# Performance work log

Hardware: AMD Instinct MI355X
Metric: run time of the kernel (lower is better)

The kernel has to match this reference:

```python
import jax, jax.numpy as jnp
import numpy as np

N = 10000        # nodes
E = 320000       # edges (before self-loops)
IN = 128         # in_channels
HID = 128        # hidden_channels per head
HEADS = 4
OUT = 512        # out_channels (final layer, 1 head, no concat)
SLOPE = 0.2      # PyG GATConv negative_slope default


def setup_inputs() -> dict:
    key = jax.random.key(0)
    ks = jax.random.split(key, 16)
    s = 0.05
    inp = {
        "x": jax.random.normal(ks[0], (N, IN), dtype=jnp.float32),
        "edge_index": jax.random.randint(ks[1], (2, E), 0, N, dtype=jnp.int32),
        # layer 1: IN -> HEADS*HID, concat
        "W1": jax.random.normal(ks[2], (IN, HEADS * HID), dtype=jnp.float32) * s,
        "a_src1": jax.random.normal(ks[3], (1, HEADS, HID), dtype=jnp.float32) * s,
        "a_dst1": jax.random.normal(ks[4], (1, HEADS, HID), dtype=jnp.float32) * s,
        "b1": jnp.zeros((HEADS * HID,), dtype=jnp.float32),
        # layer 2: HEADS*HID -> HEADS*HID, concat
        "W2": jax.random.normal(ks[5], (HEADS * HID, HEADS * HID), dtype=jnp.float32) * s,
        "a_src2": jax.random.normal(ks[6], (1, HEADS, HID), dtype=jnp.float32) * s,
        "a_dst2": jax.random.normal(ks[7], (1, HEADS, HID), dtype=jnp.float32) * s,
        "b2": jnp.zeros((HEADS * HID,), dtype=jnp.float32),
        # layer 3: HEADS*HID -> OUT, heads=1, mean (no concat)
        "W3": jax.random.normal(ks[8], (HEADS * HID, OUT), dtype=jnp.float32) * s,
        "a_src3": jax.random.normal(ks[9], (1, 1, OUT), dtype=jnp.float32) * s,
        "a_dst3": jax.random.normal(ks[10], (1, 1, OUT), dtype=jnp.float32) * s,
        "b3": jnp.zeros((OUT,), dtype=jnp.float32),
    }
    return inp


def gat_layer(x, src, dst, W, a_src, a_dst, bias, heads, ch, concat):
    n = x.shape[0]
    h = (x @ W).reshape(n, heads, ch)                 # [N,H,C]
    al_s = jnp.sum(h * a_src, axis=-1)                # [N,H]
    al_d = jnp.sum(h * a_dst, axis=-1)                # [N,H]
    logits = jax.nn.leaky_relu(al_s[src] + al_d[dst], SLOPE)  # [E,H]
    # segment softmax over incoming edges of each destination node
    logits = logits - jax.ops.segment_max(logits, dst, num_segments=n)[dst]
    e = jnp.exp(logits)
    denom = jax.ops.segment_sum(e, dst, num_segments=n)[dst]
    alpha = e / denom                                  # [E,H]
    out = jax.ops.segment_sum(h[src] * alpha[:, :, None], dst, num_segments=n)  # [N,H,C]
    out = out.reshape(n, heads * ch) if concat else out.mean(axis=1)
    return out + bias


def reference(x, edge_index, W1, a_src1, a_dst1, b1, W2, a_src2, a_dst2, b2,
              W3, a_src3, a_dst3, b3):
    n = x.shape[0]
    loop = jnp.arange(n, dtype=edge_index.dtype)       # PyG add_self_loops=True
    src = jnp.concatenate([edge_index[0], loop])
    dst = jnp.concatenate([edge_index[1], loop])
    h = jax.nn.relu(gat_layer(x, src, dst, W1, a_src1, a_dst1, b1, HEADS, HID, True))
    h = jax.nn.relu(gat_layer(h, src, dst, W2, a_src2, a_dst2, b2, HEADS, HID, True))
    return gat_layer(h, src, dst, W3, a_src3, a_dst3, b3, 1, OUT, False)
```

## Files before the change

kernel.cpp:

```cpp
#include <hip/hip_runtime.h>

#define NSLOPE 0.2f
#define CAP 128

typedef __bf16 bf16x8 __attribute__((ext_vector_type(8)));
typedef __bf16 bf16x4 __attribute__((ext_vector_type(4)));
typedef __bf16 bf16x2 __attribute__((ext_vector_type(2)));
typedef float  f32x4  __attribute__((ext_vector_type(4)));
typedef _Float16 half2v __attribute__((ext_vector_type(2)));

static __device__ __forceinline__ float dot2f(unsigned p, unsigned a, float c){
#if __has_builtin(__builtin_amdgcn_fdot2)
  return __builtin_amdgcn_fdot2(__builtin_bit_cast(half2v, p),
                                __builtin_bit_cast(half2v, a), c, false);
#else
  half2v ph = __builtin_bit_cast(half2v, p), ah = __builtin_bit_cast(half2v, a);
  return c + (float)ph[0]*(float)ah[0] + (float)ph[1]*(float)ah[1];
#endif
}


__global__ void fill_kernel(const int* __restrict__ ei, int E,
                            int* cnt, int* __restrict__ col){
  int i = blockIdx.x*blockDim.x + threadIdx.x;
  if (i < E){
    int s = ei[i], d = ei[E + i];
    int slot = atomicAdd(&cnt[d], 1);
    if (slot < CAP) col[(d << 7) + slot] = s;
  }
}

__device__ __forceinline__ void wsplit_body(
    const float* __restrict__ W, __bf16* __restrict__ Bt, int K, int Nc,
    int kb, int nb, float (*hi_s)[33]){
  int tx = threadIdx.x & 31, ty = threadIdx.x >> 5;
  int k0 = kb * 32, n0 = nb * 32;
#pragma unroll
  for (int i = 0; i < 4; i++){
    int r = ty + i*8;
    hi_s[r][tx] = (float)(__bf16)W[(size_t)(k0 + r)*Nc + n0 + tx];
  }
  __syncthreads();
  const size_t Kx16 = (size_t)K * 16;
#pragma unroll
  for (int i = 0; i < 4; i++){
    int n = ty + i*8;
    int r = n0 + n;
    size_t a = (size_t)(r >> 4)*Kx16 + (size_t)(k0 >> 5)*512
             + (size_t)((r & 15) + 16*(tx >> 3))*8 + (tx & 7);
    Bt[a] = (__bf16)hi_s[tx][n];
  }
}

__global__ __launch_bounds__(256) void prep_kernel(
    const float* __restrict__ x, __bf16* __restrict__ X2,
    const float* __restrict__ W1, __bf16* __restrict__ B1t,
    const float* __restrict__ W2, __bf16* __restrict__ B2t,
    const float* __restrict__ W3, __bf16* __restrict__ B3t,
    int* __restrict__ cnt, int* __restrict__ col,
    float* __restrict__ albase, int N){
  __shared__ float hi_s[32][33];
  int b = blockIdx.x, t = threadIdx.x;
  int gid = b*256 + t;
  if (gid < N){
    cnt[gid] = 1;
    col[gid << 7] = gid;
  }
  if (gid*4 < N*18) *(float4*)(albase + gid*4) = make_float4(0.f,0.f,0.f,0.f);

  const int nb_split = (N*32 + 255) / 256;
  if (b < nb_split){
    int i = gid * 4;
    if (i < N*128){
      int n = i >> 7, c = i & 127;
      float4 v = *(const float4*)(x + i);
      float f[4] = {v.x, v.y, v.z, v.w};
      bf16x4 h;
#pragma unroll
      for (int u = 0; u < 4; u++) h[u] = (__bf16)f[u];
      size_t a = (size_t)(n >> 4)*2048 + (size_t)(c >> 5)*512
               + (size_t)((n & 15) + 16*((c >> 3) & 3))*8 + (c & 7);
      *(bf16x4*)(X2 + a) = h;
    }
  } else if (b < nb_split + 64){
    int bb = b - nb_split;
    wsplit_body(W1, B1t, 128, 512, bb & 3, bb >> 2, hi_s);
  } else if (b < nb_split + 64 + 256){
    int bb = b - nb_split - 64;
    wsplit_body(W2, B2t, 512, 512, bb & 15, bb >> 4, hi_s);
  } else {
    int bb = b - nb_split - 320;
    wsplit_body(W3, B3t, 512, 512, bb & 15, bb >> 4, hi_s);
  }
}

template<int H>
__global__ __launch_bounds__(256) void gemm_mfma(
    const __bf16* __restrict__ A2f, const __bf16* __restrict__ B2f,
    _Float16* __restrict__ Hb, const float* __restrict__ asrc,
    const float* __restrict__ adst, float* __restrict__ al_s,
    float* __restrict__ al_d, int M, int K2){
  int t = threadIdx.x, w = t >> 6, lane = t & 63;
  int mm = lane & 15, q = lane >> 4;

  int bid = blockIdx.x;
  int idx = bid >> 3;
  int cb = idx & 3;
  int rowblk = (bid & 7) + ((idx >> 2) << 3);
  if (rowblk * 64 >= M) return;
  int bm = rowblk * 64, bn = cb * 128;
  int wr = w & 1, wc = w >> 1;

  const int nf = K2 >> 5;
  const int rbmax = (M >> 4) - 1;
  const __bf16* pA0; const __bf16* pA1;
  const __bf16* pB0; const __bf16* pB1; const __bf16* pB2; const __bf16* pB3;
  {
    int rb0 = (bm >> 4) + wr*2;     rb0 = (rb0 <= rbmax) ? rb0 : rbmax;
    int rb1 = (bm >> 4) + wr*2 + 1; rb1 = (rb1 <= rbmax) ? rb1 : rbmax;
    pA0 = A2f + (size_t)rb0*nf*512 + lane*8;
    pA1 = A2f + (size_t)rb1*nf*512 + lane*8;
    int rbB = (bn >> 4) + wc*4;
    pB0 = B2f + (size_t)(rbB+0)*nf*512 + lane*8;
    pB1 = B2f + (size_t)(rbB+1)*nf*512 + lane*8;
    pB2 = B2f + (size_t)(rbB+2)*nf*512 + lane*8;
    pB3 = B2f + (size_t)(rbB+3)*nf*512 + lane*8;
  }

  f32x4 acc[2][4];
#pragma unroll
  for (int i = 0; i < 2; i++)
#pragma unroll
    for (int j = 0; j < 4; j++)
#pragma unroll
      for (int r = 0; r < 4; r++) acc[i][j][r] = 0.f;

#pragma unroll 4
  for (int f = 0; f < nf; f++){
    bf16x8 a0 = *(const bf16x8*)(pA0 + (size_t)f*512);
    bf16x8 a1 = *(const bf16x8*)(pA1 + (size_t)f*512);
    bf16x8 b0 = *(const bf16x8*)(pB0 + (size_t)f*512);
    bf16x8 b1 = *(const bf16x8*)(pB1 + (size_t)f*512);
    bf16x8 b2 = *(const bf16x8*)(pB2 + (size_t)f*512);
    bf16x8 b3 = *(const bf16x8*)(pB3 + (size_t)f*512);
    acc[0][0] = __builtin_amdgcn_mfma_f32_16x16x32_bf16(a0, b0, acc[0][0], 0, 0, 0);
    acc[0][1] = __builtin_amdgcn_mfma_f32_16x16x32_bf16(a0, b1, acc[0][1], 0, 0, 0);
    acc[0][2] = __builtin_amdgcn_mfma_f32_16x16x32_bf16(a0, b2, acc[0][2], 0, 0, 0);
    acc[0][3] = __builtin_amdgcn_mfma_f32_16x16x32_bf16(a0, b3, acc[0][3], 0, 0, 0);
    acc[1][0] = __builtin_amdgcn_mfma_f32_16x16x32_bf16(a1, b0, acc[1][0], 0, 0, 0);
    acc[1][1] = __builtin_amdgcn_mfma_f32_16x16x32_bf16(a1, b1, acc[1][1], 0, 0, 0);
    acc[1][2] = __builtin_amdgcn_mfma_f32_16x16x32_bf16(a1, b2, acc[1][2], 0, 0, 0);
    acc[1][3] = __builtin_amdgcn_mfma_f32_16x16x32_bf16(a1, b3, acc[1][3], 0, 0, 0);
  }

  float as_v[4], ad_v[4];
#pragma unroll
  for (int j2 = 0; j2 < 4; j2++){
    int colc = bn + (wc*4 + j2)*16 + mm;
    as_v[j2] = asrc[colc];
    ad_v[j2] = adst[colc];
  }
  const int h = (H == 4) ? (bn >> 7) : 0;
#pragma unroll
  for (int i2 = 0; i2 < 2; i2++){
    int rbase = bm + (wr*2 + i2)*16 + q*4;
#pragma unroll
    for (int j2 = 0; j2 < 4; j2++){
      int colc = bn + (wc*4 + j2)*16 + mm;
#pragma unroll
      for (int r = 0; r < 4; r++){
        int row = rbase + r;
        if (row < M) Hb[(size_t)row*512 + colc] = (_Float16)acc[i2][j2][r];
      }
    }
#pragma unroll
    for (int r = 0; r < 4; r++){
      float ps = acc[i2][0][r]*as_v[0] + acc[i2][1][r]*as_v[1]
               + acc[i2][2][r]*as_v[2] + acc[i2][3][r]*as_v[3];
      float pd = acc[i2][0][r]*ad_v[0] + acc[i2][1][r]*ad_v[1]
               + acc[i2][2][r]*ad_v[2] + acc[i2][3][r]*ad_v[3];
#pragma unroll
      for (int off = 1; off < 16; off <<= 1){
        ps += __shfl_xor(ps, off);
        pd += __shfl_xor(pd, off);
      }
      int row = rbase + r;
      if (mm == 0 && row < M){
        atomicAdd(&al_s[(size_t)row*H + h], ps);
        atomicAdd(&al_d[(size_t)row*H + h], pd);
      }
    }
  }
}

template<int H, int MODE>
__global__ __launch_bounds__(256) void aggregate_slice(
    const _Float16* __restrict__ Hb, const float* __restrict__ al_s,
    const float* __restrict__ al_d, const int* __restrict__ cnt,
    const int* __restrict__ col, const float* __restrict__ bias,
    float* __restrict__ outF, __bf16* __restrict__ fA,
    int nidx, int N){
  __shared__ int      src_s[4][64];
  __shared__ _Float16 a_sh[4][64];
  int g = blockIdx.x;
  int x = g & 7, grp = g >> 3;
  int s = x >> 1, half = x & 1;
  int t = threadIdx.x, w = t >> 6, lane = t & 63;
  int dd = grp*4 + w;
  if (dd >= nidx) return;
  int d = half * nidx + dd;
  if (d >= N) return;
  const int hh = (H == 1) ? 0 : s;
  const float ald = al_d[(size_t)d*H + hh];
  int deg = cnt[d]; deg = (deg < CAP) ? deg : CAP;
  int start = d << 7;

  int sc0 = 0, sc1 = 0;
  float v0f = -1e30f, v1f = -1e30f;
  if (lane < deg){
    sc0 = col[start + lane];
    float v = al_s[(size_t)sc0*H + hh] + ald;
    v0f = (v > 0.f) ? v : NSLOPE * v;
  }
  if (64 + lane < deg){
    sc1 = col[start + 64 + lane];
    float v = al_s[(size_t)sc1*H + hh] + ald;
    v1f = (v > 0.f) ? v : NSLOPE * v;
  }
  float mx = fmaxf(v0f, v1f);
#pragma unroll
  for (int off = 32; off > 0; off >>= 1)
    mx = fmaxf(mx, __shfl_xor(mx, off));

  float e0 = (lane < deg)      ? __expf(v0f - mx) : 0.f;
  float e1 = (64 + lane < deg) ? __expf(v1f - mx) : 0.f;
  float lsum = e0 + e1;
#pragma unroll
  for (int off = 32; off > 0; off >>= 1)
    lsum += __shfl_xor(lsum, off);

  const unsigned* __restrict__ Hb32 = (const unsigned*)Hb;
  const unsigned coffu = s*64 + lane;
  float accx = 0.f, accy = 0.f;

  int cc0 = (deg < 64) ? deg : 64;
  src_s[w][lane] = sc0;
  a_sh[w][lane]  = (_Float16)e0;
  for (int chunk = 0; ; chunk++){
    int cnt2 = (chunk == 0) ? cc0 : (deg - 64);
    int npair = cnt2 >> 1;
    int j = 0;
    for (; j + 2 <= npair; j += 2){
      int s0 = src_s[w][2*j],     s1 = src_s[w][2*j+1];
      int s2 = src_s[w][2*j+2],   s3 = src_s[w][2*j+3];
      unsigned a01 = *(const unsigned*)&a_sh[w][2*j];
      unsigned a23 = *(const unsigned*)&a_sh[w][2*j+2];
      unsigned u0 = Hb32[(size_t)s0*256 + coffu];
      unsigned u1 = Hb32[(size_t)s1*256 + coffu];
      unsigned u2 = Hb32[(size_t)s2*256 + coffu];
      unsigned u3 = Hb32[(size_t)s3*256 + coffu];
      unsigned pc  = (u0 & 0x0000ffffu) | (u1 << 16);
      unsigned pc1 = (u0 >> 16) | (u1 & 0xffff0000u);
      unsigned qc  = (u2 & 0x0000ffffu) | (u3 << 16);
      unsigned qc1 = (u2 >> 16) | (u3 & 0xffff0000u);
      accx = dot2f(pc,  a01, accx);
      accy = dot2f(pc1, a01, accy);
      accx = dot2f(qc,  a23, accx);
      accy = dot2f(qc1, a23, accy);
    }
    for (; j < npair; j++){
      int s0 = src_s[w][2*j], s1 = src_s[w][2*j+1];
      unsigned a01 = *(const unsigned*)&a_sh[w][2*j];
      unsigned u0 = Hb32[(size_t)s0*256 + coffu];
      unsigned u1 = Hb32[(size_t)s1*256 + coffu];
      unsigned pc  = (u0 & 0x0000ffffu) | (u1 << 16);
      unsigned pc1 = (u0 >> 16) | (u1 & 0xffff0000u);
      accx = dot2f(pc,  a01, accx);
      accy = dot2f(pc1, a01, accy);
    }
    if (cnt2 & 1){
      int sl = src_s[w][cnt2 - 1];
      float al = (float)a_sh[w][cnt2 - 1];
      unsigned ul = Hb32[(size_t)sl*256 + coffu];
      half2v hv = __builtin_bit_cast(half2v, ul);
      accx += al * (float)hv[0];
      accy += al * (float)hv[1];
    }
    if (chunk == 1 || deg <= 64) break;
    src_s[w][lane] = sc1;
    a_sh[w][lane]  = (_Float16)e1;
  }

  float invd = 1.f / lsum;
  int c = s*128 + lane*2;
  float2 bv = *(const float2*)(bias + c);
  float r0 = accx * invd + bv.x;
  float r1 = accy * invd + bv.y;
  if (MODE == 1){
    r0 = fmaxf(r0, 0.f); r1 = fmaxf(r1, 0.f);
    bf16x2 hv; hv[0] = (__bf16)r0; hv[1] = (__bf16)r1;
    size_t a = (size_t)(d >> 4)*8192 + (size_t)(c >> 5)*512
             + (size_t)((d & 15) + 16*((c >> 3) & 3))*8 + (c & 7);
    *(bf16x2*)(fA + a) = hv;
  } else {
    *(float2*)(outF + (size_t)d*512 + c) = make_float2(r0, r1);
  }
}

extern "C" void kernel_launch(void* const* d_in, const int* in_sizes, int n_in,
                              void* d_out, int out_size, void* d_ws, size_t ws_size,
                              hipStream_t stream){
  const float* x   = (const float*)d_in[0];
  const int*   ei  = (const int*)  d_in[1];
  const float* W1  = (const float*)d_in[2];
  const float* as1 = (const float*)d_in[3];
  const float* ad1 = (const float*)d_in[4];
  const float* b1  = (const float*)d_in[5];
  const float* W2  = (const float*)d_in[6];
  const float* as2 = (const float*)d_in[7];
  const float* ad2 = (const float*)d_in[8];
  const float* b2  = (const float*)d_in[9];
  const float* W3  = (const float*)d_in[10];
  const float* as3 = (const float*)d_in[11];
  const float* ad3 = (const float*)d_in[12];
  const float* b3  = (const float*)d_in[13];
  float* out = (float*)d_out;

  const int N = in_sizes[0] / 128;
  const int E = in_sizes[1] / 2;
  const int nidx = (N + 1) / 2;

  __bf16* feat2  = (__bf16*)d_ws;
  __bf16* X2     = feat2 + (size_t)N*512;
  float*  albase = (float*)(X2 + (size_t)N*128);
  float*  als1   = albase;
  float*  ald1   = als1 + (size_t)N*4;
  float*  als2   = ald1 + (size_t)N*4;
  float*  ald2   = als2 + (size_t)N*4;
  float*  als3   = ald2 + (size_t)N*4;
  float*  ald3   = als3 + (size_t)N;
  int*    cnt    = (int*)(ald3 + (size_t)N);
  int*    col    = cnt + N;
  uintptr_t p  = (uintptr_t)(col + (size_t)N*CAP);
  p = (p + 15) & ~(uintptr_t)15;
  __bf16* B1t = (__bf16*)p;
  __bf16* B2t = B1t + 512*128;
  __bf16* B3t = B2t + 512*512;
  _Float16* Hb = (_Float16*)(B3t + 512*512);

  const int nb_split = (N*32 + 255)/256;
  const int pgrid = nb_split + 64 + 256 + 256;

  prep_kernel<<<pgrid, 256, 0, stream>>>(x, X2, W1, B1t, W2, B2t, W3, B3t,
                                         cnt, col, albase, N);
  fill_kernel<<<(E+255)/256, 256, 0, stream>>>(ei, E, cnt, col);

  const int nrb = (N + 63)/64;
  const int ggrid = (((nrb + 7) >> 3) << 3) * 4;
  const int agrid = ((nidx + 3)/4) * 8;

  gemm_mfma<4><<<ggrid, 256, 0, stream>>>(X2, B1t, Hb, as1, ad1, als1, ald1, N, 128);
  aggregate_slice<4,1><<<agrid, 256, 0, stream>>>(Hb, als1, ald1, cnt, col, b1,
      (float*)nullptr, feat2, nidx, N);

  gemm_mfma<4><<<ggrid, 256, 0, stream>>>(feat2, B2t, Hb, as2, ad2, als2, ald2, N, 512);
  aggregate_slice<4,1><<<agrid, 256, 0, stream>>>(Hb, als2, ald2, cnt, col, b2,
      (float*)nullptr, feat2, nidx, N);

  gemm_mfma<1><<<ggrid, 256, 0, stream>>>(feat2, B3t, Hb, as3, ad3, als3, ald3, N, 512);
  aggregate_slice<1,0><<<agrid, 256, 0, stream>>>(Hb, als3, ald3, cnt, col, b3,
      out, (__bf16*)nullptr, nidx, N);
}
```

Baseline: 272.6 us.

## Fuse all GAT stages into one persistent cooperative kernel with grid syncs

Replaces the eight separate kernel launches (prep, fill, three GEMM and three aggregation kernels) with a single cooperative mega-kernel. Each phase loops over virtual block indices and is separated from the next by grid.sync(). The aim is to remove launch gaps and per-kernel tail effects between the dependent stages. In exchange, occupancy is limited by the combined register and shared-memory footprint of all phases. Grid-wide barriers add cost, and the launch falls back to separate kernels if the cooperative launch fails.

```diff
diff --git a/kernel.cpp b/kernel.cpp
--- a/kernel.cpp
+++ b/kernel.cpp
@@ -1,4 +1,6 @@
 #include <hip/hip_runtime.h>
+#include <hip/hip_cooperative_groups.h>
+namespace cg = cooperative_groups;
 
 #define NSLOPE 0.2f
 #define CAP 128
@@ -20,15 +22,18 @@
 }
 
 
-__global__ void fill_kernel(const int* __restrict__ ei, int E,
-                            int* cnt, int* __restrict__ col){
-  int i = blockIdx.x*blockDim.x + threadIdx.x;
-  if (i < E){
-    int s = ei[i], d = ei[E + i];
-    int slot = atomicAdd(&cnt[d], 1);
-    if (slot < CAP) col[(d << 7) + slot] = s;
-  }
-}
+struct MegaP {
+  const float* x; const int* ei;
+  const float* W1; const float* as1; const float* ad1; const float* b1;
+  const float* W2; const float* as2; const float* ad2; const float* b2;
+  const float* W3; const float* as3; const float* ad3; const float* b3;
+  float* out;
+  __bf16* feat2; __bf16* X2; float* albase;
+  float* als1; float* ald1; float* als2; float* ald2; float* als3; float* ald3;
+  int* cnt; int* col;
+  __bf16* B1t; __bf16* B2t; __bf16* B3t; _Float16* Hb;
+  int N, E, nidx;
+};
 
 __device__ __forceinline__ void wsplit_body(
     const float* __restrict__ W, __bf16* __restrict__ Bt, int K, int Nc,
@@ -52,58 +57,60 @@
   }
 }
 
-__global__ __launch_bounds__(256) void prep_kernel(
-    const float* __restrict__ x, __bf16* __restrict__ X2,
-    const float* __restrict__ W1, __bf16* __restrict__ B1t,
-    const float* __restrict__ W2, __bf16* __restrict__ B2t,
-    const float* __restrict__ W3, __bf16* __restrict__ B3t,
-    int* __restrict__ cnt, int* __restrict__ col,
-    float* __restrict__ albase, int N){
-  __shared__ float hi_s[32][33];
-  int b = blockIdx.x, t = threadIdx.x;
+__device__ __forceinline__ void prep_body(int b, int t, const MegaP& p,
+                                          float (*hi_s)[33]){
+  const int N = p.N;
   int gid = b*256 + t;
   if (gid < N){
-    cnt[gid] = 1;
-    col[gid << 7] = gid;
-  }
-  if (gid*4 < N*18) *(float4*)(albase + gid*4) = make_float4(0.f,0.f,0.f,0.f);
+    p.cnt[gid] = 1;
+    p.col[gid << 7] = gid;
+  }
+  if (gid*4 < N*18) *(float4*)(p.albase + gid*4) = make_float4(0.f,0.f,0.f,0.f);
 
   const int nb_split = (N*32 + 255) / 256;
   if (b < nb_split){
     int i = gid * 4;
     if (i < N*128){
       int n = i >> 7, c = i & 127;
-      float4 v = *(const float4*)(x + i);
+      float4 v = *(const float4*)(p.x + i);
       float f[4] = {v.x, v.y, v.z, v.w};
       bf16x4 h;
 #pragma unroll
       for (int u = 0; u < 4; u++) h[u] = (__bf16)f[u];
       size_t a = (size_t)(n >> 4)*2048 + (size_t)(c >> 5)*512
                + (size_t)((n & 15) + 16*((c >> 3) & 3))*8 + (c & 7);
-      *(bf16x4*)(X2 + a) = h;
+      *(bf16x4*)(p.X2 + a) = h;
     }
   } else if (b < nb_split + 64){
     int bb = b - nb_split;
-    wsplit_body(W1, B1t, 128, 512, bb & 3, bb >> 2, hi_s);
+    wsplit_body(p.W1, p.B1t, 128, 512, bb & 3, bb >> 2, hi_s);
   } else if (b < nb_split + 64 + 256){
     int bb = b - nb_split - 64;
-    wsplit_body(W2, B2t, 512, 512, bb & 15, bb >> 4, hi_s);
-  } else {
+    wsplit_body(p.W2, p.B2t, 512, 512, bb & 15, bb >> 4, hi_s);
+  } else if (b < nb_split + 64 + 512){
     int bb = b - nb_split - 320;
-    wsplit_body(W3, B3t, 512, 512, bb & 15, bb >> 4, hi_s);
+    wsplit_body(p.W3, p.B3t, 512, 512, bb & 15, bb >> 4, hi_s);
+  }
+}
+
+__device__ __forceinline__ void fill_body(int b, int t, const MegaP& p){
+  int i = b*256 + t;
+  if (i < p.E){
+    int s = p.ei[i], d = p.ei[p.E + i];
+    int slot = atomicAdd(&p.cnt[d], 1);
+    if (slot < CAP) p.col[(d << 7) + slot] = s;
   }
 }
 
 template<int H>
-__global__ __launch_bounds__(256) void gemm_mfma(
+__device__ __forceinline__ void gemm_body(int bid, int t,
     const __bf16* __restrict__ A2f, const __bf16* __restrict__ B2f,
     _Float16* __restrict__ Hb, const float* __restrict__ asrc,
     const float* __restrict__ adst, float* __restrict__ al_s,
     float* __restrict__ al_d, int M, int K2){
-  int t = threadIdx.x, w = t >> 6, lane = t & 63;
+  int w = t >> 6, lane = t & 63;
   int mm = lane & 15, q = lane >> 4;
 
-  int bid = blockIdx.x;
   int idx = bid >> 3;
   int cb = idx & 3;
   int rowblk = (bid & 7) + ((idx >> 2) << 3);
@@ -194,18 +201,15 @@
 }
 
 template<int H, int MODE>
-__global__ __launch_bounds__(256) void aggregate_slice(
+__device__ __forceinline__ void agg_body(int g, int t,
     const _Float16* __restrict__ Hb, const float* __restrict__ al_s,
     const float* __restrict__ al_d, const int* __restrict__ cnt,
     const int* __restrict__ col, const float* __restrict__ bias,
-    float* __restrict__ outF, __bf16* __restrict__ fA,
-    int nidx, int N){
-  __shared__ int      src_s[4][64];
-  __shared__ _Float16 a_sh[4][64];
-  int g = blockIdx.x;
+    float* __restrict__ outF, __bf16* __restrict__ fA, int nidx, int N,
+    int (*src_s)[64], _Float16 (*a_sh)[64]){
   int x = g & 7, grp = g >> 3;
   int s = x >> 1, half = x & 1;
-  int t = threadIdx.x, w = t >> 6, lane = t & 63;
+  int w = t >> 6, lane = t & 63;
   int dd = grp*4 + w;
   if (dd >= nidx) return;
   int d = half * nidx + dd;
@@ -307,25 +311,79 @@
   }
 }
 
+__global__ __launch_bounds__(256) void mega(MegaP p){
+  cg::grid_group grid = cg::this_grid();
+  __shared__ float hi_s[32][33];
+  __shared__ int src_s[4][64];
+  __shared__ _Float16 a_sh[4][64];
+  const int G = gridDim.x, b0 = blockIdx.x, t = threadIdx.x;
+  const int N = p.N, E = p.E, nidx = p.nidx;
+
+  const int nb_split = (N*32 + 255)/256;
+  const int pgrid = nb_split + 64 + 256 + 256;
+  for (int b = b0; b < pgrid; b += G){
+    prep_body(b, t, p, hi_s);
+    __syncthreads();
+  }
+  grid.sync();
+  const int fgrid = (E + 255)/256;
+  for (int b = b0; b < fgrid; b += G) fill_body(b, t, p);
+  grid.sync();
+
+  const int nrb = (N + 63)/64;
+  const int ggrid = (((nrb + 7) >> 3) << 3) * 4;
+  const int agrid = ((nidx + 3)/4) * 8;
+
+  for (int b = b0; b < ggrid; b += G)
+    gemm_body<4>(b, t, p.X2, p.B1t, p.Hb, p.as1, p.ad1, p.als1, p.ald1, N, 128);
+  grid.sync();
+  for (int b = b0; b < agrid; b += G)
+    agg_body<4,1>(b, t, p.Hb, p.als1, p.ald1, p.cnt, p.col, p.b1,
+                  (float*)nullptr, p.feat2, nidx, N, src_s, a_sh);
+  grid.sync();
+  for (int b = b0; b < ggrid; b += G)
+    gemm_body<4>(b, t, p.feat2, p.B2t, p.Hb, p.as2, p.ad2, p.als2, p.ald2, N, 512);
+  grid.sync();
+  for (int b = b0; b < agrid; b += G)
+    agg_body<4,1>(b, t, p.Hb, p.als2, p.ald2, p.cnt, p.col, p.b2,
+                  (float*)nullptr, p.feat2, nidx, N, src_s, a_sh);
+  grid.sync();
+  for (int b = b0; b < ggrid; b += G)
+    gemm_body<1>(b, t, p.feat2, p.B3t, p.Hb, p.as3, p.ad3, p.als3, p.ald3, N, 512);
+  grid.sync();
+  for (int b = b0; b < agrid; b += G)
+    agg_body<1,0>(b, t, p.Hb, p.als3, p.ald3, p.cnt, p.col, p.b3,
+                  p.out, (__bf16*)nullptr, nidx, N, src_s, a_sh);
+}
+
+__global__ __launch_bounds__(256) void prep_kernel(MegaP p){
+  __shared__ float hi_s[32][33];
+  prep_body(blockIdx.x, threadIdx.x, p, hi_s);
+}
+__global__ void fill_kernel(MegaP p){
+  fill_body(blockIdx.x, threadIdx.x, p);
+}
+template<int H>
+__global__ __launch_bounds__(256) void gemm_k(
+    const __bf16* A2f, const __bf16* B2f, _Float16* Hb,
+    const float* asrc, const float* adst, float* al_s, float* al_d,
+    int M, int K2){
+  gemm_body<H>(blockIdx.x, threadIdx.x, A2f, B2f, Hb, asrc, adst, al_s, al_d, M, K2);
+}
+template<int H, int MODE>
+__global__ __launch_bounds__(256) void agg_k(
+    const _Float16* Hb, const float* al_s, const float* al_d,
+    const int* cnt, const int* col, const float* bias,
+    float* outF, __bf16* fA, int nidx, int N){
+  __shared__ int src_s[4][64];
+  __shared__ _Float16 a_sh[4][64];
+  agg_body<H,MODE>(blockIdx.x, threadIdx.x, Hb, al_s, al_d, cnt, col, bias,
+                   outF, fA, nidx, N, src_s, a_sh);
+}
+
 extern "C" void kernel_launch(void* const* d_in, const int* in_sizes, int n_in,
                               void* d_out, int out_size, void* d_ws, size_t ws_size,
                               hipStream_t stream){
-  const float* x   = (const float*)d_in[0];
-  const int*   ei  = (const int*)  d_in[1];
-  const float* W1  = (const float*)d_in[2];
-  const float* as1 = (const float*)d_in[3];
-  const float* ad1 = (const float*)d_in[4];
-  const float* b1  = (const float*)d_in[5];
-  const float* W2  = (const float*)d_in[6];
-  const float* as2 = (const float*)d_in[7];
-  const float* ad2 = (const float*)d_in[8];
-  const float* b2  = (const float*)d_in[9];
-  const float* W3  = (const float*)d_in[10];
-  const float* as3 = (const float*)d_in[11];
-  const float* ad3 = (const float*)d_in[12];
-  const float* b3  = (const float*)d_in[13];
-  float* out = (float*)d_out;
-
   const int N = in_sizes[0] / 128;
   const int E = in_sizes[1] / 2;
   const int nidx = (N + 1) / 2;
@@ -341,33 +399,58 @@
   float*  ald3   = als3 + (size_t)N;
   int*    cnt    = (int*)(ald3 + (size_t)N);
   int*    col    = cnt + N;
-  uintptr_t p  = (uintptr_t)(col + (size_t)N*CAP);
-  p = (p + 15) & ~(uintptr_t)15;
-  __bf16* B1t = (__bf16*)p;
+  uintptr_t pa = (uintptr_t)(col + (size_t)N*CAP);
+  pa = (pa + 15) & ~(uintptr_t)15;
+  __bf16* B1t = (__bf16*)pa;
   __bf16* B2t = B1t + 512*128;
   __bf16* B3t = B2t + 512*512;
   _Float16* Hb = (_Float16*)(B3t + 512*512);
 
-  const int nb_split = (N*32 + 255)/256;
-  const int pgrid = nb_split + 64 + 256 + 256;
-
-  prep_kernel<<<pgrid, 256, 0, stream>>>(x, X2, W1, B1t, W2, B2t, W3, B3t,
-                                         cnt, col, albase, N);
-  fill_kernel<<<(E+255)/256, 256, 0, stream>>>(ei, E, cnt, col);
-
-  const int nrb = (N + 63)/64;
-  const int ggrid = (((nrb + 7) >> 3) << 3) * 4;
-  const int agrid = ((nidx + 3)/4) * 8;
-
-  gemm_mfma<4><<<ggrid, 256, 0, stream>>>(X2, B1t, Hb, as1, ad1, als1, ald1, N, 128);
-  aggregate_slice<4,1><<<agrid, 256, 0, stream>>>(Hb, als1, ald1, cnt, col, b1,
-      (float*)nullptr, feat2, nidx, N);
-
-  gemm_mfma<4><<<ggrid, 256, 0, stream>>>(feat2, B2t, Hb, as2, ad2, als2, ald2, N, 512);
-  aggregate_slice<4,1><<<agrid, 256, 0, stream>>>(Hb, als2, ald2, cnt, col, b2,
-      (float*)nullptr, feat2, nidx, N);
-
-  gemm_mfma<1><<<ggrid, 256, 0, stream>>>(feat2, B3t, Hb, as3, ad3, als3, ald3, N, 512);
-  aggregate_slice<1,0><<<agrid, 256, 0, stream>>>(Hb, als3, ald3, cnt, col, b3,
-      out, (__bf16*)nullptr, nidx, N);
-}
+  MegaP P;
+  P.x = (const float*)d_in[0];   P.ei = (const int*)d_in[1];
+  P.W1 = (const float*)d_in[2];  P.as1 = (const float*)d_in[3];
+  P.ad1 = (const float*)d_in[4]; P.b1 = (const float*)d_in[5];
+  P.W2 = (const float*)d_in[6];  P.as2 = (const float*)d_in[7];
+  P.ad2 = (const float*)d_in[8]; P.b2 = (const float*)d_in[9];
+  P.W3 = (const float*)d_in[10]; P.as3 = (const float*)d_in[11];
+  P.ad3 = (const float*)d_in[12]; P.b3 = (const float*)d_in[13];
+  P.out = (float*)d_out;
+  P.feat2 = feat2; P.X2 = X2; P.albase = albase;
+  P.als1 = als1; P.ald1 = ald1; P.als2 = als2; P.ald2 = ald2;
+  P.als3 = als3; P.ald3 = ald3;
+  P.cnt = cnt; P.col = col;
+  P.B1t = B1t; P.B2t = B2t; P.B3t = B3t; P.Hb = Hb;
+  P.N = N; P.E = E; P.nidx = nidx;
+
+  int maxb = 0;
+  hipError_t oe = hipOccupancyMaxActiveBlocksPerMultiprocessor(
+      &maxb, reinterpret_cast<const void*>(mega), 256, 0);
+  if (oe != hipSuccess || maxb < 1) maxb = 2;
+  long Gl = (long)maxb * 256;
+  if (Gl > 2048) Gl = 2048;
+  int G = (int)(Gl & ~7L);
+  if (G < 256) G = 256;
+
+  void* kargs[] = { &P };
+  hipError_t le = hipLaunchCooperativeKernel(
+      reinterpret_cast<const void*>(mega), dim3(G), dim3(256), kargs, 0, stream);
+
+  if (le != hipSuccess){
+    const int nb_split = (N*32 + 255)/256;
+    const int pgrid = nb_split + 64 + 256 + 256;
+    prep_kernel<<<pgrid, 256, 0, stream>>>(P);
+    fill_kernel<<<(E+255)/256, 256, 0, stream>>>(P);
+    const int nrb = (N + 63)/64;
+    const int ggrid = (((nrb + 7) >> 3) << 3) * 4;
+    const int agrid = ((nidx + 3)/4) * 8;
+    gemm_k<4><<<ggrid, 256, 0, stream>>>(X2, B1t, Hb, P.as1, P.ad1, als1, ald1, N, 128);
+    agg_k<4,1><<<agrid, 256, 0, stream>>>(Hb, als1, ald1, cnt, col, P.b1,
+        (float*)nullptr, feat2, nidx, N);
+    gemm_k<4><<<ggrid, 256, 0, stream>>>(feat2, B2t, Hb, P.as2, P.ad2, als2, ald2, N, 512);
+    agg_k<4,1><<<agrid, 256, 0, stream>>>(Hb, als2, ald2, cnt, col, P.b2,
+        (float*)nullptr, feat2, nidx, N);
+    gemm_k<1><<<ggrid, 256, 0, stream>>>(feat2, B3t, Hb, P.as3, P.ad3, als3, ald3, N, 512);
+    agg_k<1,0><<<agrid, 256, 0, stream>>>(Hb, als3, ald3, cnt, col, P.b3,
+        P.out, (__bf16*)nullptr, nidx, N);
+  }
+}
```

Result: slower. 873.1 us (+220.3%).

## Split each destination's edge list across four waves with block-level reduction

Applied to the files above, without the earlier changes.

The aggregation kernel now assigns one destination node (and head slice) per block instead of one per wave. Its edge list is divided into four quarters, one per wave, and the softmax max/sum and the accumulators are combined through shared memory with __syncthreads. Source indices and exp weights are broadcast with shuffles instead of LDS arrays, and the weights are packed to fp16 on the fly. The goal is to cut per-wave serial latency over the ~33 edges per node and raise memory-level parallelism. In exchange it launches four times as many blocks, adds barriers, and leaves three of the four waves idle in the epilogue.

```diff
diff --git a/kernel.cpp b/kernel.cpp
--- a/kernel.cpp
+++ b/kernel.cpp
@@ -16,6 +16,15 @@
 #else
   half2v ph = __builtin_bit_cast(half2v, p), ah = __builtin_bit_cast(half2v, a);
   return c + (float)ph[0]*(float)ah[0] + (float)ph[1]*(float)ah[1];
+#endif
+}
+
+static __device__ __forceinline__ unsigned pk2h(float a, float b){
+#if __has_builtin(__builtin_amdgcn_cvt_pkrtz)
+  return __builtin_bit_cast(unsigned, __builtin_amdgcn_cvt_pkrtz(a, b));
+#else
+  half2v h; h[0] = (_Float16)a; h[1] = (_Float16)b;
+  return __builtin_bit_cast(unsigned, h);
 #endif
 }
 
@@ -200,110 +209,105 @@
     const int* __restrict__ col, const float* __restrict__ bias,
     float* __restrict__ outF, __bf16* __restrict__ fA,
     int nidx, int N){
-  __shared__ int      src_s[4][64];
-  __shared__ _Float16 a_sh[4][64];
+  __shared__ float red[8];
+  __shared__ float partx[4][64], party[4][64];
   int g = blockIdx.x;
-  int x = g & 7, grp = g >> 3;
+  int x = g & 7, idx = g >> 3;
   int s = x >> 1, half = x & 1;
+  int d = half * nidx + idx;
+  if (d >= N) return;
   int t = threadIdx.x, w = t >> 6, lane = t & 63;
-  int dd = grp*4 + w;
-  if (dd >= nidx) return;
-  int d = half * nidx + dd;
-  if (d >= N) return;
   const int hh = (H == 1) ? 0 : s;
   const float ald = al_d[(size_t)d*H + hh];
   int deg = cnt[d]; deg = (deg < CAP) ? deg : CAP;
   int start = d << 7;
-
-  int sc0 = 0, sc1 = 0;
-  float v0f = -1e30f, v1f = -1e30f;
-  if (lane < deg){
-    sc0 = col[start + lane];
-    float v = al_s[(size_t)sc0*H + hh] + ald;
-    v0f = (v > 0.f) ? v : NSLOPE * v;
-  }
-  if (64 + lane < deg){
-    sc1 = col[start + 64 + lane];
-    float v = al_s[(size_t)sc1*H + hh] + ald;
-    v1f = (v > 0.f) ? v : NSLOPE * v;
-  }
-  float mx = fmaxf(v0f, v1f);
+  int qlen = (deg + 3) >> 2;
+  int qbeg = w * qlen;
+  int qcnt = deg - qbeg;
+  qcnt = (qcnt < 0) ? 0 : ((qcnt < qlen) ? qcnt : qlen);
+
+  int sc = 0; float vf = -1e30f;
+  if (lane < qcnt){
+    sc = col[start + qbeg + lane];
+    float v = al_s[(size_t)sc*H + hh] + ald;
+    vf = (v > 0.f) ? v : NSLOPE * v;
+  }
+  float mx = vf;
 #pragma unroll
   for (int off = 32; off > 0; off >>= 1)
     mx = fmaxf(mx, __shfl_xor(mx, off));
-
-  float e0 = (lane < deg)      ? __expf(v0f - mx) : 0.f;
-  float e1 = (64 + lane < deg) ? __expf(v1f - mx) : 0.f;
-  float lsum = e0 + e1;
+  if (lane == 0) red[w] = mx;
+  __syncthreads();
+  mx = fmaxf(fmaxf(red[0], red[1]), fmaxf(red[2], red[3]));
+  float e = (lane < qcnt) ? __expf(vf - mx) : 0.f;
+  float ss = e;
 #pragma unroll
   for (int off = 32; off > 0; off >>= 1)
-    lsum += __shfl_xor(lsum, off);
+    ss += __shfl_xor(ss, off);
+  if (lane == 0) red[4 + w] = ss;
+  __syncthreads();
+  float lsum = (red[4] + red[5]) + (red[6] + red[7]);
 
   const unsigned* __restrict__ Hb32 = (const unsigned*)Hb;
   const unsigned coffu = s*64 + lane;
   float accx = 0.f, accy = 0.f;
 
-  int cc0 = (deg < 64) ? deg : 64;
-  src_s[w][lane] = sc0;
-  a_sh[w][lane]  = (_Float16)e0;
-  for (int chunk = 0; ; chunk++){
-    int cnt2 = (chunk == 0) ? cc0 : (deg - 64);
-    int npair = cnt2 >> 1;
-    int j = 0;
-    for (; j + 2 <= npair; j += 2){
-      int s0 = src_s[w][2*j],     s1 = src_s[w][2*j+1];
-      int s2 = src_s[w][2*j+2],   s3 = src_s[w][2*j+3];
-      unsigned a01 = *(const unsigned*)&a_sh[w][2*j];
-      unsigned a23 = *(const unsigned*)&a_sh[w][2*j+2];
-      unsigned u0 = Hb32[(size_t)s0*256 + coffu];
-      unsigned u1 = Hb32[(size_t)s1*256 + coffu];
-      unsigned u2 = Hb32[(size_t)s2*256 + coffu];
-      unsigned u3 = Hb32[(size_t)s3*256 + coffu];
-      unsigned pc  = (u0 & 0x0000ffffu) | (u1 << 16);
-      unsigned pc1 = (u0 >> 16) | (u1 & 0xffff0000u);
-      unsigned qc  = (u2 & 0x0000ffffu) | (u3 << 16);
-      unsigned qc1 = (u2 >> 16) | (u3 & 0xffff0000u);
-      accx = dot2f(pc,  a01, accx);
-      accy = dot2f(pc1, a01, accy);
-      accx = dot2f(qc,  a23, accx);
-      accy = dot2f(qc1, a23, accy);
+  int npc = (qcnt + 1) >> 1;
+  int j = 0;
+  for (; j + 2 <= npc; j += 2){
+    int s0 = __shfl(sc, 2*j),   s1 = __shfl(sc, 2*j+1);
+    int s2 = __shfl(sc, 2*j+2), s3 = __shfl(sc, 2*j+3);
+    float f0 = __shfl(e, 2*j),   f1 = __shfl(e, 2*j+1);
+    float f2 = __shfl(e, 2*j+2), f3 = __shfl(e, 2*j+3);
+    unsigned u0 = Hb32[(size_t)s0*256 + coffu];
+    unsigned u1 = Hb32[(size_t)s1*256 + coffu];
+    unsigned u2 = Hb32[(size_t)s2*256 + coffu];
+    unsigned u3 = Hb32[(size_t)s3*256 + coffu];
+    unsigned a01 = pk2h(f0, f1);
+    unsigned a23 = pk2h(f2, f3);
+    unsigned pc  = (u0 & 0x0000ffffu) | (u1 << 16);
+    unsigned pc1 = (u0 >> 16) | (u1 & 0xffff0000u);
+    unsigned qc  = (u2 & 0x0000ffffu) | (u3 << 16);
+    unsigned qc1 = (u2 >> 16) | (u3 & 0xffff0000u);
+    accx = dot2f(pc,  a01, accx);
+    accy = dot2f(pc1, a01, accy);
+    accx = dot2f(qc,  a23, accx);
+    accy = dot2f(qc1, a23, accy);
+  }
+  for (; j < npc; j++){
+    int s0 = __shfl(sc, 2*j), s1 = __shfl(sc, 2*j+1);
+    float f0 = __shfl(e, 2*j), f1 = __shfl(e, 2*j+1);
+    unsigned u0 = Hb32[(size_t)s0*256 + coffu];
+    unsigned u1 = Hb32[(size_t)s1*256 + coffu];
+    unsigned a01 = pk2h(f0, f1);
+    unsigned pc  = (u0 & 0x0000ffffu) | (u1 << 16);
+    unsigned pc1 = (u0 >> 16) | (u1 & 0xffff0000u);
+    accx = dot2f(pc,  a01, accx);
+    accy = dot2f(pc1, a01, accy);
+  }
+
+  partx[w][lane] = accx;
+  party[w][lane] = accy;
+  __syncthreads();
+  if (w == 0){
+    float ax = (partx[0][lane] + partx[1][lane])
+             + (partx[2][lane] + partx[3][lane]);
+    float ay = (party[0][lane] + party[1][lane])
+             + (party[2][lane] + party[3][lane]);
+    float invd = 1.f / lsum;
+    int c = s*128 + lane*2;
+    float2 bv = *(const float2*)(bias + c);
+    float r0 = ax * invd + bv.x;
+    float r1 = ay * invd + bv.y;
+    if (MODE == 1){
+      r0 = fmaxf(r0, 0.f); r1 = fmaxf(r1, 0.f);
+      bf16x2 hv; hv[0] = (__bf16)r0; hv[1] = (__bf16)r1;
+      size_t a = (size_t)(d >> 4)*8192 + (size_t)(c >> 5)*512
+               + (size_t)((d & 15) + 16*((c >> 3) & 3))*8 + (c & 7);
+      *(bf16x2*)(fA + a) = hv;
+    } else {
+      *(float2*)(outF + (size_t)d*512 + c) = make_float2(r0, r1);
     }
-    for (; j < npair; j++){
-      int s0 = src_s[w][2*j], s1 = src_s[w][2*j+1];
-      unsigned a01 = *(const unsigned*)&a_sh[w][2*j];
-      unsigned u0 = Hb32[(size_t)s0*256 + coffu];
-      unsigned u1 = Hb32[(size_t)s1*256 + coffu];
-      unsigned pc  = (u0 & 0x0000ffffu) | (u1 << 16);
-      unsigned pc1 = (u0 >> 16) | (u1 & 0xffff0000u);
-      accx = dot2f(pc,  a01, accx);
-      accy = dot2f(pc1, a01, accy);
-    }
-    if (cnt2 & 1){
-      int sl = src_s[w][cnt2 - 1];
-      float al = (float)a_sh[w][cnt2 - 1];
-      unsigned ul = Hb32[(size_t)sl*256 + coffu];
-      half2v hv = __builtin_bit_cast(half2v, ul);
-      accx += al * (float)hv[0];
-      accy += al * (float)hv[1];
-    }
-    if (chunk == 1 || deg <= 64) break;
-    src_s[w][lane] = sc1;
-    a_sh[w][lane]  = (_Float16)e1;
-  }
-
-  float invd = 1.f / lsum;
-  int c = s*128 + lane*2;
-  float2 bv = *(const float2*)(bias + c);
-  float r0 = accx * invd + bv.x;
-  float r1 = accy * invd + bv.y;
-  if (MODE == 1){
-    r0 = fmaxf(r0, 0.f); r1 = fmaxf(r1, 0.f);
-    bf16x2 hv; hv[0] = (__bf16)r0; hv[1] = (__bf16)r1;
-    size_t a = (size_t)(d >> 4)*8192 + (size_t)(c >> 5)*512
-             + (size_t)((d & 15) + 16*((c >> 3) & 3))*8 + (c & 7);
-    *(bf16x2*)(fA + a) = hv;
-  } else {
-    *(float2*)(outF + (size_t)d*512 + c) = make_float2(r0, r1);
   }
 }
 
@@ -357,7 +361,7 @@
 
   const int nrb = (N + 63)/64;
   const int ggrid = (((nrb + 7) >> 3) << 3) * 4;
-  const int agrid = ((nidx + 3)/4) * 8;
+  const int agrid = nidx * 8;
 
   gemm_mfma<4><<<ggrid, 256, 0, stream>>>(X2, B1t, Hb, as1, ad1, als1, ald1, N, 128);
   aggregate_slice<4,1><<<agrid, 256, 0, stream>>>(Hb, als1, ald1, cnt, col, b1,
```

After: 371.4 us. +36.3%, slower.
